# Optimization experiments

Hardware: AMD Instinct MI355X
Metric: run time of the kernel (lower is better)

The kernel has to match this reference:

```python
import jax, jax.numpy as jnp
from jax import lax
import numpy as np

B, D_IN, L, D, K, DS = 8, 16, 4096, 512, 4, 4
BLOCKS = (1, 2, 3, 4)          # block sizes, all offset 0 (max_block_size=4)
PAD_MULT = 12                  # lcm(1,2,3,4)


def setup_inputs() -> dict:
    key = jax.random.key(0)
    ks = jax.random.split(key, 5)
    return {
        "x": jax.random.normal(ks[0], (B, D_IN, L), jnp.float32),
        "conv_w": jax.random.normal(ks[1], (D, D_IN, K), jnp.float32) * 0.05,
        "conv_b": jax.random.normal(ks[2], (D,), jnp.float32) * 0.02,
        "score_w": jax.random.normal(ks[3], (D,), jnp.float32) * 0.02,
        "score_b": jax.random.normal(ks[4], (1,), jnp.float32) * 0.02,
    }


def reference(x, conv_w, conv_b, score_w, score_b):
    # pos_conv: Conv1d(padding='same', k=4). Torch 'same' with even kernel pads
    # left=(k-1)//2=1, right=2.
    h = lax.conv_general_dilated(x, conv_w, (1,), [(1, 2)],
                                 dimension_numbers=('NCH', 'OIH', 'NCH'))
    h = jnp.transpose(h, (0, 2, 1)) + conv_b            # [B, L, D]

    Np = -(-L // PAD_MULT) * PAD_MULT                   # pad seq to multiple of 12
    h = jnp.pad(h, ((0, 0), (0, Np - L), (0, 0)))       # [B, Np, D]

    # per-block-size mean pooling, then broadcast back to char resolution
    reprs = []
    for m in BLOCKS:
        r = h.reshape(B, Np // m, m, D).mean(axis=2)    # [B, Np/m, D]
        reprs.append(jnp.repeat(r, m, axis=1))          # [B, Np, D]
    br = jnp.stack(reprs, axis=2)                       # [B, Np, nb, D]

    # score each block representation, softmax over block sizes
    scores = jnp.einsum('bnmd,d->bnm', br, score_w) + score_b[0]
    scores = jax.nn.softmax(scores, axis=2)             # [B, Np, nb]

    # consensus attention across positions over the nb-dim score vectors
    sim = jnp.einsum('bim,bjm->bij', scores, scores)    # [B, Np, Np]
    attn = jax.nn.softmax(sim, axis=-1)
    scores = jnp.einsum('bij,bjm->bim', attn, scores)   # [B, Np, nb]

    # weighted sum of block reprs
    xo = jnp.einsum('bnmd,bnm->bnd', br, scores)        # [B, Np, D]

    mlen = -(-L // DS) * DS                              # 4096 (== L here)
    char_x = xo[:, :mlen]
    xd = char_x.reshape(B, mlen // DS, DS, D).mean(axis=2)  # [B, L/DS, D]
    return char_x[:, :L], xd
```

## Files before the change

kernel.cpp:

```cpp
#include <hip/hip_runtime.h>
#include <hip/hip_bf16.h>

#define B_ 8
#define DIN 16
#define L_ 4096
#define D_ 512
#define NP 4104
#define NG 342
#define JSP 32
#define JCH 129
#define SPAN2 96
#define NSPAN2 43
#define XSTR 104

__device__ __forceinline__ unsigned short f2bf(float f) {
  unsigned int u = __float_as_uint(f);
  unsigned int r = (u + 0x7fffu + ((u >> 16) & 1u)) >> 16;
  return (unsigned short)r;
}
__device__ __forceinline__ float bf2f(unsigned int u) {
  return __uint_as_float(u << 16);
}

__device__ __constant__ float D5[6] = {0.9999544f, 1.0005163f, 0.4975827f,
                                       0.1726558f, 0.0334570f, 0.0140872f};
__device__ __constant__ float FACT[6] = {1.f, 1.f, 2.f, 6.f, 24.f, 120.f};

__global__ __launch_bounds__(256) void k_uprep(
    const float* __restrict__ cw, const float* __restrict__ cb,
    const float* __restrict__ sw, float* __restrict__ us) {
  __shared__ float red[4][64];
  __shared__ float red2[64];
  int t = threadIdx.x;
  int p = t & 63, chunk = t >> 6;
  float s = 0.f;
  for (int d = chunk * 128; d < chunk * 128 + 128; ++d)
    s = fmaf(sw[d], cw[((size_t)d << 6) + p], s);
  red[chunk][p] = s;
  if (t < 64) {
    float pc = 0.f;
    for (int j = 0; j < 8; ++j) pc = fmaf(sw[t + 64 * j], cb[t + 64 * j], pc);
    red2[t] = pc;
  }
  __syncthreads();
  if (t < 64) us[t] = red[0][t] + red[1][t] + red[2][t] + red[3][t];
  if (t == 0) {
    float c0 = 0.f;
    for (int j = 0; j < 64; ++j) c0 += red2[j];
    us[64] = c0;
  }
}

__global__ __launch_bounds__(192) void k_scores(
    const float* __restrict__ x, const float* __restrict__ us,
    const float* __restrict__ sb, unsigned short* __restrict__ s0) {
  __shared__ float xs[DIN * 195];
  __shared__ float ul[65];
  __shared__ float tb[192];
  int bid = blockIdx.x;
  int b = bid / 22, blk = bid - b * 22;
  int base0 = blk * 192;
  int t = threadIdx.x;
  const float* xb = x + (size_t)b * DIN * L_;
  for (int q = t; q < DIN * 195; q += 192) {
    int i = q / 195, c = q - i * 195;
    int nx = base0 - 1 + c;
    xs[q] = (nx >= 0 && nx < L_) ? xb[i * L_ + nx] : 0.f;
  }
  if (t < 65) ul[t] = us[t];
  __syncthreads();
  int n = base0 + t;
  float tv = 0.f;
  if (n < L_) {
    tv = ul[64];
    for (int i = 0; i < DIN; ++i) {
#pragma unroll
      for (int k = 0; k < 4; ++k)
        tv = fmaf(xs[i * 195 + t + k], ul[(i << 2) + k], tv);
    }
  }
  tb[t] = tv;
  __syncthreads();
  if (n < NP) {
    float t1 = tb[t];
    int e2 = t & ~1;
    float t2 = 0.5f * (tb[e2] + tb[e2 + 1]);
    int e3 = (t / 3) * 3;
    float t3 = (1.f / 3.f) * (tb[e3] + tb[e3 + 1] + tb[e3 + 2]);
    int e4 = t & ~3;
    float t4 = 0.25f * (tb[e4] + tb[e4 + 1] + tb[e4 + 2] + tb[e4 + 3]);
    float sbv = sb[0];
    float c0s = t1 + sbv, c1s = t2 + sbv, c2s = t3 + sbv, c3s = t4 + sbv;
    float mx = fmaxf(fmaxf(c0s, c1s), fmaxf(c2s, c3s));
    float e0 = __expf(c0s - mx), e1 = __expf(c1s - mx);
    float e2f = __expf(c2s - mx), e3f = __expf(c3s - mx);
    float inv = 1.f / (e0 + e1 + e2f + e3f);
    ushort4 ov;
    ov.x = f2bf(e0 * inv); ov.y = f2bf(e1 * inv);
    ov.z = f2bf(e2f * inv); ov.w = f2bf(e3f * inv);
    *reinterpret_cast<ushort4*>(&s0[(((size_t)b * NP) + n) << 2]) = ov;
  }
}

__global__ __launch_bounds__(256) void k_moment(
    const unsigned short* __restrict__ s0, float* __restrict__ Mpart) {
  __shared__ float sv[JCH][4];
  __shared__ float ls[JCH][4];
  __shared__ float mp[4][128][5];
  int bid = blockIdx.x;
  int js = bid & 31;
  int b = bid >> 5;
  int t = threadIdx.x;
  int lane = t & 63, wv = t >> 6;
  int jlo = js * JCH;
  int cnt = NP - jlo; if (cnt > JCH) cnt = JCH;

  const ushort4* sp = reinterpret_cast<const ushort4*>(s0) + (size_t)b * NP + jlo;
  for (int r = t; r < cnt; r += 256) {
    ushort4 u = sp[r];
    float v0 = bf2f(u.x), v1 = bf2f(u.y), v2 = bf2f(u.z), v3 = bf2f(u.w);
    sv[r][0] = v0; sv[r][1] = v1; sv[r][2] = v2; sv[r][3] = v3;
    ls[r][0] = __log2f(v0); ls[r][1] = __log2f(v1);
    ls[r][2] = __log2f(v2); ls[r][3] = __log2f(v3);
  }
  int f1 = lane, f2 = lane + 64;
  float e1a = 0.f, e1b = 0.f, e1c = 0.f, e1d = 0.f;
  float e2a = 0.f, e2b = 0.f, e2c = 0.f, e2d = 0.f;
  {
    int f = 0;
    for (int a = 0; a <= 5; ++a)
      for (int b2 = 0; b2 <= 5 - a; ++b2)
        for (int c = 0; c <= 5 - a - b2; ++c)
          for (int d2 = 0; d2 <= 5 - a - b2 - c; ++d2) {
            if (f == f1) { e1a = a; e1b = b2; e1c = c; e1d = d2; }
            if (f == f2) { e2a = a; e2b = b2; e2c = c; e2d = d2; }
            ++f;
          }
  }
  __syncthreads();
  float acc1[5] = {0.f, 0.f, 0.f, 0.f, 0.f};
  float acc2[5] = {0.f, 0.f, 0.f, 0.f, 0.f};
  for (int jj = wv; jj < cnt; jj += 4) {
    float4 lv = *reinterpret_cast<float4*>(&ls[jj][0]);
    float4 vv = *reinterpret_cast<float4*>(&sv[jj][0]);
    float t1 = e1a * lv.x;
    t1 = fmaf(e1b, lv.y, t1);
    t1 = fmaf(e1c, lv.z, t1);
    t1 = fmaf(e1d, lv.w, t1);
    float t2 = e2a * lv.x;
    t2 = fmaf(e2b, lv.y, t2);
    t2 = fmaf(e2c, lv.z, t2);
    t2 = fmaf(e2d, lv.w, t2);
    float m1 = exp2f(t1);
    float m2 = exp2f(t2);
    acc1[0] = fmaf(m1, vv.x, acc1[0]);
    acc1[1] = fmaf(m1, vv.y, acc1[1]);
    acc1[2] = fmaf(m1, vv.z, acc1[2]);
    acc1[3] = fmaf(m1, vv.w, acc1[3]);
    acc1[4] += m1;
    acc2[0] = fmaf(m2, vv.x, acc2[0]);
    acc2[1] = fmaf(m2, vv.y, acc2[1]);
    acc2[2] = fmaf(m2, vv.z, acc2[2]);
    acc2[3] = fmaf(m2, vv.w, acc2[3]);
    acc2[4] += m2;
  }
#pragma unroll
  for (int c = 0; c < 5; ++c) {
    mp[wv][lane][c] = acc1[c];
    mp[wv][lane + 64][c] = acc2[c];
  }
  __syncthreads();
  if (t < 630) {
    int f = t / 5, c = t - f * 5;
    float s = mp[0][f][c] + mp[1][f][c] + mp[2][f][c] + mp[3][f][c];
    Mpart[((size_t)(b * 32 + js)) * 640 + t] = s;
  }
}

__global__ __launch_bounds__(640) void k_mred(
    const float* __restrict__ Mpart, float* __restrict__ Mfin) {
  int b = blockIdx.x;
  int t = threadIdx.x;
  if (t >= 630) return;
  int f = t / 5, c = t - f * 5;
  float s = 0.f;
  for (int js = 0; js < JSP; ++js)
    s += Mpart[((size_t)(b * 32 + js)) * 640 + t];
  int fa = 0, fb = 0, fc = 0, fd = 0;
  {
    int ff = 0;
    for (int a = 0; a <= 5; ++a)
      for (int b2 = 0; b2 <= 5 - a; ++b2)
        for (int cc = 0; cc <= 5 - a - b2; ++cc)
          for (int d2 = 0; d2 <= 5 - a - b2 - cc; ++d2) {
            if (ff == f) { fa = a; fb = b2; fc = cc; fd = d2; }
            ++ff;
          }
  }
  int k = fa + fb + fc + fd;
  float w = D5[k] * FACT[k] / (FACT[fa] * FACT[fb] * FACT[fc] * FACT[fd]);
  Mfin[((size_t)b * 128 + f) * 8 + c] = w * s;
}

__global__ __launch_bounds__(256) void k_apply(
    const unsigned short* __restrict__ s0, const float* __restrict__ Mfin,
    float* __restrict__ s2) {
  __shared__ float M[128 * 8];
  int bid = blockIdx.x;
  int b = bid / 17, ch = bid - b * 17;
  int t = threadIdx.x;
  const float4* Mb = reinterpret_cast<const float4*>(Mfin + (size_t)b * 128 * 8);
  if (t < 252) *reinterpret_cast<float4*>(&M[t * 4]) = Mb[t];
  __syncthreads();
  int i = ch * 256 + t;
  if (i >= NP) return;
  ushort4 u = reinterpret_cast<const ushort4*>(s0)[(size_t)b * NP + i];
  float s_0 = bf2f(u.x), s_1 = bf2f(u.y), s_2 = bf2f(u.z), s_3 = bf2f(u.w);
  float a0 = 0.f, a1 = 0.f, a2 = 0.f, a3 = 0.f, az = 0.f;
  int f = 0;
  float pa = 1.f;
#pragma unroll
  for (int a = 0; a <= 5; ++a) {
    float pb = pa;
#pragma unroll
    for (int b2 = 0; b2 <= 5 - a; ++b2) {
      float pc = pb;
#pragma unroll
      for (int c = 0; c <= 5 - a - b2; ++c) {
        float run = pc;
#pragma unroll
        for (int d2 = 0; d2 <= 5 - a - b2 - c; ++d2) {
          const float* mf = &M[f * 8];
          float4 m4 = *reinterpret_cast<const float4*>(mf);
          a0 = fmaf(run, m4.x, a0);
          a1 = fmaf(run, m4.y, a1);
          a2 = fmaf(run, m4.z, a2);
          a3 = fmaf(run, m4.w, a3);
          az = fmaf(run, mf[4], az);
          run *= s_3;
          ++f;
        }
        pc *= s_2;
      }
      pb *= s_1;
    }
    pa *= s_0;
  }
  float inv = 1.f / az;
  reinterpret_cast<float4*>(s2)[(size_t)b * NP + i] =
      make_float4(a0 * inv, a1 * inv, a2 * inv, a3 * inv);
}

__global__ __launch_bounds__(256, 4) void k_fused(
    const float* __restrict__ x, const float* __restrict__ cw,
    const float* __restrict__ cb, const float* __restrict__ s2,
    float* __restrict__ out) {
  __shared__ float ws_w[32 * 132];
  __shared__ float ws_x[DIN * XSTR];
  __shared__ float ss[8][12][4];
  int bid = blockIdx.x;
  int dtile = bid & 7;
  int span = (bid >> 3) % NSPAN2;
  int b = bid / (8 * NSPAN2);
  int n0 = span * SPAN2;
  int d0 = dtile * 64;
  int g0 = n0 / 12;
  int tid = threadIdx.x;

  for (int q = tid; q < 64 * 16; q += 256) {
    int dd = q >> 4, qq = (q & 15) << 2;
    float4 wv = *reinterpret_cast<const float4*>(cw + ((size_t)(d0 + dd) << 6) + qq);
    *reinterpret_cast<float4*>(&ws_w[(dd >> 1) * 132 + (dd & 1) * 64 + qq]) = wv;
  }
  const float* xb = x + (size_t)b * DIN * L_;
  for (int q = tid; q < DIN * XSTR; q += 256) {
    int i = q / XSTR, c = q - i * XSTR;
    int nx = n0 - 1 + c;
    ws_x[q] = (c < 99 && nx >= 0 && nx < L_) ? xb[i * L_ + nx] : 0.f;
  }
  for (int q = tid; q < 384; q += 256) {
    int gg = q / 48, r = q - gg * 48;
    int g = g0 + gg;
    ((float*)ss)[q] = (g < NG) ? s2[((size_t)b * NP + g * 12) * 4 + r] : 0.f;
  }
  __syncthreads();

  int dp = tid & 31;
  int seg = tid >> 5;
  int g = g0 + seg;
  float acc0[12], acc1[12];
#pragma unroll
  for (int j = 0; j < 12; ++j) { acc0[j] = 0.f; acc1[j] = 0.f; }

  for (int i = 0; i < DIN; ++i) {
    const float* wp = &ws_w[dp * 132 + (i << 2)];
    float4 wv0 = *reinterpret_cast<const float4*>(wp);
    float4 wv1 = *reinterpret_cast<const float4*>(wp + 64);
    const float* xp = &ws_x[i * XSTR + seg * 12];
    float4 xv0 = *reinterpret_cast<const float4*>(xp);
    float4 xv1 = *reinterpret_cast<const float4*>(xp + 4);
    float4 xv2 = *reinterpret_cast<const float4*>(xp + 8);
    float4 xv3 = *reinterpret_cast<const float4*>(xp + 12);
    float xr[16] = {xv0.x, xv0.y, xv0.z, xv0.w, xv1.x, xv1.y, xv1.z, xv1.w,
                    xv2.x, xv2.y, xv2.z, xv2.w, xv3.x, xv3.y, xv3.z, xv3.w};
#pragma unroll
    for (int j = 0; j < 12; ++j) {
      float a0 = acc0[j], a1 = acc1[j];
      a0 = fmaf(wv0.x, xr[j], a0);
      a0 = fmaf(wv0.y, xr[j + 1], a0);
      a0 = fmaf(wv0.z, xr[j + 2], a0);
      a0 = fmaf(wv0.w, xr[j + 3], a0);
      a1 = fmaf(wv1.x, xr[j], a1);
      a1 = fmaf(wv1.y, xr[j + 1], a1);
      a1 = fmaf(wv1.z, xr[j + 2], a1);
      a1 = fmaf(wv1.w, xr[j + 3], a1);
      acc0[j] = a0; acc1[j] = a1;
    }
  }
  if (g >= NG) return;

  int d = d0 + (dp << 1);
  float cb0 = cb[d], cb1 = cb[d + 1];
  int base = g * 12;
  float hv0[12], hv1[12];
#pragma unroll
  for (int j = 0; j < 12; ++j) {
    int n = base + j;
    if (n < L_) { hv0[j] = acc0[j] + cb0; hv1[j] = acc1[j] + cb1; }
    else { hv0[j] = 0.f; hv1[j] = 0.f; }
  }
  float P20[6], P21[6], P30[4], P31[4], P40[3], P41[3];
#pragma unroll
  for (int q = 0; q < 6; ++q) {
    P20[q] = 0.5f * (hv0[2 * q] + hv0[2 * q + 1]);
    P21[q] = 0.5f * (hv1[2 * q] + hv1[2 * q + 1]);
  }
#pragma unroll
  for (int q = 0; q < 4; ++q) {
    P30[q] = (1.f / 3.f) * (hv0[3 * q] + hv0[3 * q + 1] + hv0[3 * q + 2]);
    P31[q] = (1.f / 3.f) * (hv1[3 * q] + hv1[3 * q + 1] + hv1[3 * q + 2]);
  }
#pragma unroll
  for (int q = 0; q < 3; ++q) {
    P40[q] = 0.25f * (hv0[4 * q] + hv0[4 * q + 1] + hv0[4 * q + 2] + hv0[4 * q + 3]);
    P41[q] = 0.25f * (hv1[4 * q] + hv1[4 * q + 1] + hv1[4 * q + 2] + hv1[4 * q + 3]);
  }
  float* outc = out;
  float* outd = out + (size_t)B_ * L_ * D_;
  float xq0[3] = {0.f, 0.f, 0.f}, xq1[3] = {0.f, 0.f, 0.f};
#pragma unroll
  for (int j = 0; j < 12; ++j) {
    float w0 = ss[seg][j][0], w1 = ss[seg][j][1];
    float w2 = ss[seg][j][2], w3 = ss[seg][j][3];
    float v0 = w0 * hv0[j] + w1 * P20[j >> 1] + w2 * P30[j / 3] + w3 * P40[j >> 2];
    float v1 = w0 * hv1[j] + w1 * P21[j >> 1] + w2 * P31[j / 3] + w3 * P41[j >> 2];
    int n = base + j;
    if (n < L_) {
      float2 o; o.x = v0; o.y = v1;
      *reinterpret_cast<float2*>(&outc[((size_t)b * L_ + n) * D_ + d]) = o;
    }
    xq0[j >> 2] += v0; xq1[j >> 2] += v1;
  }
#pragma unroll
  for (int q = 0; q < 3; ++q) {
    int r = 3 * g + q;
    if (r < 1024) {
      float2 o; o.x = 0.25f * xq0[q]; o.y = 0.25f * xq1[q];
      *reinterpret_cast<float2*>(&outd[((size_t)b * 1024 + r) * D_ + d]) = o;
    }
  }
}

extern "C" void kernel_launch(void* const* d_in, const int* in_sizes, int n_in,
                              void* d_out, int out_size, void* d_ws, size_t ws_size,
                              hipStream_t stream) {
  const float* x = (const float*)d_in[0];
  const float* cw = (const float*)d_in[1];
  const float* cb = (const float*)d_in[2];
  const float* sw = (const float*)d_in[3];
  const float* sb = (const float*)d_in[4];
  float* out = (float*)d_out;
  char* ws = (char*)d_ws;
  size_t off = 0;
  unsigned short* s0 = (unsigned short*)(ws + off);
  off += 262656;
  float* s2 = (float*)(ws + off);
  off += 525312;
  float* Mpart = (float*)(ws + off);
  off += 655360;
  float* Mfin = (float*)(ws + off);
  off += 32768;
  float* us = (float*)(ws + off);

  k_uprep<<<1, 256, 0, stream>>>(cw, cb, sw, us);
  k_scores<<<8 * 22, 192, 0, stream>>>(x, us, sb, s0);
  k_moment<<<B_ * JSP, 256, 0, stream>>>(s0, Mpart);
  k_mred<<<B_, 640, 0, stream>>>(Mpart, Mfin);
  k_apply<<<B_ * 17, 256, 0, stream>>>(s0, Mfin, s2);
  k_fused<<<B_ * NSPAN2 * 8, 256, 0, stream>>>(x, cw, cb, s2, out);
}
```

Measured before the change: 77.74 us.

## Fuse score prep, scoring and moment accumulation into one kernel; fold reduction into apply

Merges the projection-vector prep, score softmax and moment partial sums into a single kernel. Each block recomputes the score-weight projection redundantly and emits moment partials computed from its own 192 positions. The final partial-sum reduction and weighting move into k_apply, which removes three kernel launches and their global round-trips. The cost is redundant projection work in every block, plus a longer 44-way reduction repeated by every apply block.

```diff
diff --git a/kernel.cpp b/kernel.cpp
--- a/kernel.cpp
+++ b/kernel.cpp
@@ -7,8 +7,7 @@
 #define D_ 512
 #define NP 4104
 #define NG 342
-#define JSP 32
-#define JCH 129
+#define NCH 44
 #define SPAN2 96
 #define NSPAN2 43
 #define XSTR 104
@@ -26,191 +25,145 @@
                                        0.1726558f, 0.0334570f, 0.0140872f};
 __device__ __constant__ float FACT[6] = {1.f, 1.f, 2.f, 6.f, 24.f, 120.f};
 
-__global__ __launch_bounds__(256) void k_uprep(
-    const float* __restrict__ cw, const float* __restrict__ cb,
-    const float* __restrict__ sw, float* __restrict__ us) {
-  __shared__ float red[4][64];
-  __shared__ float red2[64];
-  int t = threadIdx.x;
-  int p = t & 63, chunk = t >> 6;
-  float s = 0.f;
-  for (int d = chunk * 128; d < chunk * 128 + 128; ++d)
-    s = fmaf(sw[d], cw[((size_t)d << 6) + p], s);
-  red[chunk][p] = s;
-  if (t < 64) {
-    float pc = 0.f;
-    for (int j = 0; j < 8; ++j) pc = fmaf(sw[t + 64 * j], cb[t + 64 * j], pc);
-    red2[t] = pc;
-  }
-  __syncthreads();
-  if (t < 64) us[t] = red[0][t] + red[1][t] + red[2][t] + red[3][t];
-  if (t == 0) {
-    float c0 = 0.f;
-    for (int j = 0; j < 64; ++j) c0 += red2[j];
-    us[64] = c0;
-  }
-}
-
-__global__ __launch_bounds__(192) void k_scores(
-    const float* __restrict__ x, const float* __restrict__ us,
-    const float* __restrict__ sb, unsigned short* __restrict__ s0) {
+__global__ __launch_bounds__(256) void k_scores2(
+    const float* __restrict__ x, const float* __restrict__ cw,
+    const float* __restrict__ cb, const float* __restrict__ sw,
+    const float* __restrict__ sb, unsigned short* __restrict__ s0,
+    float* __restrict__ Mpart) {
   __shared__ float xs[DIN * 195];
+  __shared__ float ured[4][65];
   __shared__ float ul[65];
   __shared__ float tb[192];
+  __shared__ __align__(16) float sval[192][5];
+  __shared__ __align__(16) float lsv[192][4];
   int bid = blockIdx.x;
   int b = bid / 22, blk = bid - b * 22;
   int base0 = blk * 192;
   int t = threadIdx.x;
+
   const float* xb = x + (size_t)b * DIN * L_;
-  for (int q = t; q < DIN * 195; q += 192) {
+  for (int q = t; q < DIN * 195; q += 256) {
     int i = q / 195, c = q - i * 195;
     int nx = base0 - 1 + c;
     xs[q] = (nx >= 0 && nx < L_) ? xb[i * L_ + nx] : 0.f;
   }
-  if (t < 65) ul[t] = us[t];
-  __syncthreads();
-  int n = base0 + t;
-  float tv = 0.f;
-  if (n < L_) {
-    tv = ul[64];
-    for (int i = 0; i < DIN; ++i) {
-#pragma unroll
-      for (int k = 0; k < 4; ++k)
-        tv = fmaf(xs[i * 195 + t + k], ul[(i << 2) + k], tv);
-    }
-  }
-  tb[t] = tv;
-  __syncthreads();
-  if (n < NP) {
-    float t1 = tb[t];
-    int e2 = t & ~1;
-    float t2 = 0.5f * (tb[e2] + tb[e2 + 1]);
-    int e3 = (t / 3) * 3;
-    float t3 = (1.f / 3.f) * (tb[e3] + tb[e3 + 1] + tb[e3 + 2]);
-    int e4 = t & ~3;
-    float t4 = 0.25f * (tb[e4] + tb[e4 + 1] + tb[e4 + 2] + tb[e4 + 3]);
-    float sbv = sb[0];
-    float c0s = t1 + sbv, c1s = t2 + sbv, c2s = t3 + sbv, c3s = t4 + sbv;
-    float mx = fmaxf(fmaxf(c0s, c1s), fmaxf(c2s, c3s));
-    float e0 = __expf(c0s - mx), e1 = __expf(c1s - mx);
-    float e2f = __expf(c2s - mx), e3f = __expf(c3s - mx);
-    float inv = 1.f / (e0 + e1 + e2f + e3f);
-    ushort4 ov;
-    ov.x = f2bf(e0 * inv); ov.y = f2bf(e1 * inv);
-    ov.z = f2bf(e2f * inv); ov.w = f2bf(e3f * inv);
-    *reinterpret_cast<ushort4*>(&s0[(((size_t)b * NP) + n) << 2]) = ov;
-  }
-}
-
-__global__ __launch_bounds__(256) void k_moment(
-    const unsigned short* __restrict__ s0, float* __restrict__ Mpart) {
-  __shared__ float sv[JCH][4];
-  __shared__ float ls[JCH][4];
-  __shared__ float mp[4][128][5];
-  int bid = blockIdx.x;
-  int js = bid & 31;
-  int b = bid >> 5;
-  int t = threadIdx.x;
-  int lane = t & 63, wv = t >> 6;
-  int jlo = js * JCH;
-  int cnt = NP - jlo; if (cnt > JCH) cnt = JCH;
-
-  const ushort4* sp = reinterpret_cast<const ushort4*>(s0) + (size_t)b * NP + jlo;
-  for (int r = t; r < cnt; r += 256) {
-    ushort4 u = sp[r];
-    float v0 = bf2f(u.x), v1 = bf2f(u.y), v2 = bf2f(u.z), v3 = bf2f(u.w);
-    sv[r][0] = v0; sv[r][1] = v1; sv[r][2] = v2; sv[r][3] = v3;
-    ls[r][0] = __log2f(v0); ls[r][1] = __log2f(v1);
-    ls[r][2] = __log2f(v2); ls[r][3] = __log2f(v3);
-  }
-  int f1 = lane, f2 = lane + 64;
-  float e1a = 0.f, e1b = 0.f, e1c = 0.f, e1d = 0.f;
-  float e2a = 0.f, e2b = 0.f, e2c = 0.f, e2d = 0.f;
   {
-    int f = 0;
-    for (int a = 0; a <= 5; ++a)
-      for (int b2 = 0; b2 <= 5 - a; ++b2)
-        for (int c = 0; c <= 5 - a - b2; ++c)
-          for (int d2 = 0; d2 <= 5 - a - b2 - c; ++d2) {
-            if (f == f1) { e1a = a; e1b = b2; e1c = c; e1d = d2; }
-            if (f == f2) { e2a = a; e2b = b2; e2c = c; e2d = d2; }
-            ++f;
-          }
-  }
-  __syncthreads();
-  float acc1[5] = {0.f, 0.f, 0.f, 0.f, 0.f};
-  float acc2[5] = {0.f, 0.f, 0.f, 0.f, 0.f};
-  for (int jj = wv; jj < cnt; jj += 4) {
-    float4 lv = *reinterpret_cast<float4*>(&ls[jj][0]);
-    float4 vv = *reinterpret_cast<float4*>(&sv[jj][0]);
-    float t1 = e1a * lv.x;
-    t1 = fmaf(e1b, lv.y, t1);
-    t1 = fmaf(e1c, lv.z, t1);
-    t1 = fmaf(e1d, lv.w, t1);
-    float t2 = e2a * lv.x;
-    t2 = fmaf(e2b, lv.y, t2);
-    t2 = fmaf(e2c, lv.z, t2);
-    t2 = fmaf(e2d, lv.w, t2);
-    float m1 = exp2f(t1);
-    float m2 = exp2f(t2);
-    acc1[0] = fmaf(m1, vv.x, acc1[0]);
-    acc1[1] = fmaf(m1, vv.y, acc1[1]);
-    acc1[2] = fmaf(m1, vv.z, acc1[2]);
-    acc1[3] = fmaf(m1, vv.w, acc1[3]);
-    acc1[4] += m1;
-    acc2[0] = fmaf(m2, vv.x, acc2[0]);
-    acc2[1] = fmaf(m2, vv.y, acc2[1]);
-    acc2[2] = fmaf(m2, vv.z, acc2[2]);
-    acc2[3] = fmaf(m2, vv.w, acc2[3]);
-    acc2[4] += m2;
-  }
-#pragma unroll
-  for (int c = 0; c < 5; ++c) {
-    mp[wv][lane][c] = acc1[c];
-    mp[wv][lane + 64][c] = acc2[c];
-  }
-  __syncthreads();
-  if (t < 630) {
-    int f = t / 5, c = t - f * 5;
-    float s = mp[0][f][c] + mp[1][f][c] + mp[2][f][c] + mp[3][f][c];
-    Mpart[((size_t)(b * 32 + js)) * 640 + t] = s;
-  }
-}
-
-__global__ __launch_bounds__(640) void k_mred(
-    const float* __restrict__ Mpart, float* __restrict__ Mfin) {
-  int b = blockIdx.x;
-  int t = threadIdx.x;
-  if (t >= 630) return;
-  int f = t / 5, c = t - f * 5;
-  float s = 0.f;
-  for (int js = 0; js < JSP; ++js)
-    s += Mpart[((size_t)(b * 32 + js)) * 640 + t];
-  int fa = 0, fb = 0, fc = 0, fd = 0;
-  {
-    int ff = 0;
-    for (int a = 0; a <= 5; ++a)
-      for (int b2 = 0; b2 <= 5 - a; ++b2)
-        for (int cc = 0; cc <= 5 - a - b2; ++cc)
-          for (int d2 = 0; d2 <= 5 - a - b2 - cc; ++d2) {
-            if (ff == f) { fa = a; fb = b2; fc = cc; fd = d2; }
-            ++ff;
-          }
-  }
-  int k = fa + fb + fc + fd;
-  float w = D5[k] * FACT[k] / (FACT[fa] * FACT[fb] * FACT[fc] * FACT[fd]);
-  Mfin[((size_t)b * 128 + f) * 8 + c] = w * s;
+    int lane = t & 63, wv = t >> 6;
+    float ua = 0.f, ca = 0.f;
+    for (int d = wv * 128; d < wv * 128 + 128; ++d) {
+      ua = fmaf(sw[d], cw[((size_t)d << 6) + lane], ua);
+      ca = fmaf(sw[d], cb[d], ca);
+    }
+    ured[wv][lane] = ua;
+    if (lane == 0) ured[wv][64] = ca;
+  }
+  __syncthreads();
+  if (t < 65) ul[t] = ured[0][t] + ured[1][t] + ured[2][t] + ured[3][t];
+  __syncthreads();
+
+  if (t < 192) {
+    int n = base0 + t;
+    float tv = 0.f;
+    if (n < L_) {
+      tv = ul[64];
+      for (int i = 0; i < DIN; ++i) {
+#pragma unroll
+        for (int k = 0; k < 4; ++k)
+          tv = fmaf(xs[i * 195 + t + k], ul[(i << 2) + k], tv);
+      }
+    }
+    tb[t] = tv;
+  }
+  __syncthreads();
+
+  if (t < 192) {
+    int n = base0 + t;
+    if (n < NP) {
+      float t1 = tb[t];
+      int e2 = t & ~1;
+      float t2 = 0.5f * (tb[e2] + tb[e2 + 1]);
+      int e3 = (t / 3) * 3;
+      float t3 = (1.f / 3.f) * (tb[e3] + tb[e3 + 1] + tb[e3 + 2]);
+      int e4 = t & ~3;
+      float t4 = 0.25f * (tb[e4] + tb[e4 + 1] + tb[e4 + 2] + tb[e4 + 3]);
+      float sbv = sb[0];
+      float c0s = t1 + sbv, c1s = t2 + sbv, c2s = t3 + sbv, c3s = t4 + sbv;
+      float mx = fmaxf(fmaxf(c0s, c1s), fmaxf(c2s, c3s));
+      float e0 = __expf(c0s - mx), e1 = __expf(c1s - mx);
+      float e2f = __expf(c2s - mx), e3f = __expf(c3s - mx);
+      float inv = 1.f / (e0 + e1 + e2f + e3f);
+      float v0 = e0 * inv, v1 = e1 * inv, v2 = e2f * inv, v3 = e3f * inv;
+      ushort4 ov;
+      ov.x = f2bf(v0); ov.y = f2bf(v1); ov.z = f2bf(v2); ov.w = f2bf(v3);
+      *reinterpret_cast<ushort4*>(&s0[(((size_t)b * NP) + n) << 2]) = ov;
+      sval[t][0] = v0; sval[t][1] = v1; sval[t][2] = v2; sval[t][3] = v3;
+      sval[t][4] = 1.f;
+      lsv[t][0] = __log2f(v0); lsv[t][1] = __log2f(v1);
+      lsv[t][2] = __log2f(v2); lsv[t][3] = __log2f(v3);
+    } else {
+      sval[t][0] = 0.f; sval[t][1] = 0.f; sval[t][2] = 0.f;
+      sval[t][3] = 0.f; sval[t][4] = 0.f;
+      lsv[t][0] = 0.f; lsv[t][1] = 0.f; lsv[t][2] = 0.f; lsv[t][3] = 0.f;
+    }
+  }
+  __syncthreads();
+
+  int half = (t >= 128) ? 1 : 0;
+  int f = t - half * 128;
+  if (f < 126) {
+    int fa = 0, fb = 0, fc = 0, fd = 0;
+    {
+      int ff = 0;
+      for (int a = 0; a <= 5; ++a)
+        for (int b2 = 0; b2 <= 5 - a; ++b2)
+          for (int cc = 0; cc <= 5 - a - b2; ++cc)
+            for (int d2 = 0; d2 <= 5 - a - b2 - cc; ++d2) {
+              if (ff == f) { fa = a; fb = b2; fc = cc; fd = d2; }
+              ++ff;
+            }
+    }
+    float ea = (float)fa, eb = (float)fb, ec = (float)fc, ed = (float)fd;
+    int k = fa + fb + fc + fd;
+    float w = D5[k] * FACT[k] / (FACT[fa] * FACT[fb] * FACT[fc] * FACT[fd]);
+    float a0 = 0.f, a1 = 0.f, a2 = 0.f, a3 = 0.f, a4 = 0.f;
+    int r0 = half * 96;
+    for (int r = r0; r < r0 + 96; ++r) {
+      float4 lv = *reinterpret_cast<const float4*>(&lsv[r][0]);
+      float dot = ea * lv.x;
+      dot = fmaf(eb, lv.y, dot);
+      dot = fmaf(ec, lv.z, dot);
+      dot = fmaf(ed, lv.w, dot);
+      float m = exp2f(dot);
+      a0 = fmaf(m, sval[r][0], a0);
+      a1 = fmaf(m, sval[r][1], a1);
+      a2 = fmaf(m, sval[r][2], a2);
+      a3 = fmaf(m, sval[r][3], a3);
+      a4 = fmaf(m, sval[r][4], a4);
+    }
+    size_t pbase = ((size_t)(b * NCH + blk * 2 + half)) * 640 + f * 5;
+    Mpart[pbase + 0] = w * a0;
+    Mpart[pbase + 1] = w * a1;
+    Mpart[pbase + 2] = w * a2;
+    Mpart[pbase + 3] = w * a3;
+    Mpart[pbase + 4] = w * a4;
+  }
 }
 
 __global__ __launch_bounds__(256) void k_apply(
-    const unsigned short* __restrict__ s0, const float* __restrict__ Mfin,
+    const unsigned short* __restrict__ s0, const float* __restrict__ Mpart,
     float* __restrict__ s2) {
   __shared__ float M[128 * 8];
   int bid = blockIdx.x;
   int b = bid / 17, ch = bid - b * 17;
   int t = threadIdx.x;
-  const float4* Mb = reinterpret_cast<const float4*>(Mfin + (size_t)b * 128 * 8);
-  if (t < 252) *reinterpret_cast<float4*>(&M[t * 4]) = Mb[t];
+  for (int e = t; e < 630; e += 256) {
+    float s = 0.f;
+#pragma unroll 4
+    for (int c2 = 0; c2 < NCH; ++c2)
+      s += Mpart[((size_t)(b * NCH + c2)) * 640 + e];
+    int f = e / 5, c = e - f * 5;
+    M[f * 8 + c] = s;
+  }
   __syncthreads();
   int i = ch * 256 + t;
   if (i >= NP) return;
@@ -387,15 +340,9 @@
   float* s2 = (float*)(ws + off);
   off += 525312;
   float* Mpart = (float*)(ws + off);
-  off += 655360;
-  float* Mfin = (float*)(ws + off);
-  off += 32768;
-  float* us = (float*)(ws + off);
-
-  k_uprep<<<1, 256, 0, stream>>>(cw, cb, sw, us);
-  k_scores<<<8 * 22, 192, 0, stream>>>(x, us, sb, s0);
-  k_moment<<<B_ * JSP, 256, 0, stream>>>(s0, Mpart);
-  k_mred<<<B_, 640, 0, stream>>>(Mpart, Mfin);
-  k_apply<<<B_ * 17, 256, 0, stream>>>(s0, Mfin, s2);
+  off += 901120;
+
+  k_scores2<<<8 * 22, 256, 0, stream>>>(x, cw, cb, sw, sb, s0, Mpart);
+  k_apply<<<8 * 17, 256, 0, stream>>>(s0, Mpart, s2);
   k_fused<<<B_ * NSPAN2 * 8, 256, 0, stream>>>(x, cw, cb, s2, out);
 }
```

Result: no change. 77.34 us (-0.5%).
